# Kernel optimization log

Hardware: AMD Instinct MI355X
Metric: run time of the kernel (lower is better)

Reference implementation:

```python
import jax, jax.numpy as jnp
import numpy as np

N_NODES = 50000
N_EDGES = 400000
D = 256
EDGE_DIM = 64
N_LAYERS = 3


def setup_inputs() -> dict:
    key = jax.random.key(0)
    ks = jax.random.split(key, 8)
    sc = 1.0 / np.sqrt(D)
    x = jax.random.normal(ks[0], (N_NODES, D), dtype=jnp.float32)
    edge_attr = jax.random.normal(ks[1], (N_EDGES, EDGE_DIM), dtype=jnp.float32)
    edge_index = jax.random.randint(ks[2], (2, N_EDGES), 0, N_NODES, dtype=jnp.int64)
    Wl = jax.random.normal(ks[3], (N_LAYERS, D, D), dtype=jnp.float32) * sc
    bl = jax.random.normal(ks[4], (N_LAYERS, D), dtype=jnp.float32) * 0.01
    Wr = jax.random.normal(ks[5], (N_LAYERS, D, D), dtype=jnp.float32) * sc
    We = jax.random.normal(ks[6], (N_LAYERS, D, EDGE_DIM), dtype=jnp.float32) * (1.0 / np.sqrt(EDGE_DIM))
    be = jax.random.normal(ks[7], (N_LAYERS, D), dtype=jnp.float32) * 0.01
    return {"x": x, "edge_attr": edge_attr, "edge_index": edge_index,
            "Wl": Wl, "bl": bl, "Wr": Wr, "We": We, "be": be}


def reference(x, edge_attr, edge_index, Wl, bl, Wr, We, be):
    # SAGEConv (mean aggr, root_weight=True, no normalize) with edge-feature
    # augmented messages: msg = x[src] + edge_lin(edge_attr)
    src, dst = edge_index[0], edge_index[1]
    n = x.shape[0]
    # per-target in-degree for mean aggregation (computed once; edge_index fixed)
    deg = jax.ops.segment_sum(jnp.ones((edge_index.shape[1],), x.dtype), dst,
                              num_segments=n)
    inv_deg = (1.0 / jnp.maximum(deg, 1.0))[:, None]  # [N,1]
    for l in range(Wl.shape[0]):
        e_msg = edge_attr @ We[l].T + be[l]                 # [E,D] edge_lin
        msg = x[src] + e_msg                                 # gather + add
        agg = jax.ops.segment_sum(msg, dst, num_segments=n) * inv_deg  # mean
        x = jax.nn.relu(agg @ Wl[l].T + bl[l] + x @ Wr[l].T)
    return x
```

## Files before the change

kernel.cpp:

```cpp
#include <hip/hip_runtime.h>

typedef __attribute__((ext_vector_type(8))) short bf16x8;
typedef __attribute__((ext_vector_type(4))) float f32x4;
typedef unsigned short u16;

__device__ __forceinline__ u16 f2bf(float f) {
    union { float f; unsigned u; } v; v.f = f;
    unsigned u = v.u;
    return (u16)((u + 0x7FFFu + ((u >> 16) & 1u)) >> 16);
}
__device__ __forceinline__ float bf2f(u16 h) {
    union { unsigned u; float f; } v; v.u = ((unsigned)h) << 16;
    return v.f;
}

__global__ __launch_bounds__(256) void k_convert(const float* __restrict__ x,
                                                 u16* __restrict__ hb, int total4) {
    int i = blockIdx.x * 256 + threadIdx.x;
    if (i >= total4) return;
    float4 v = ((const float4*)x)[i];
    ushort4 o;
    o.x = f2bf(v.x); o.y = f2bf(v.y); o.z = f2bf(v.z); o.w = f2bf(v.w);
    ((ushort4*)hb)[i] = o;
}

__global__ __launch_bounds__(256) void k_count(const int* __restrict__ dst,
                                               int* __restrict__ deg, int E) {
    int e = blockIdx.x * 256 + threadIdx.x;
    if (e < E) atomicAdd(&deg[dst[e]], 1);
}

__global__ __launch_bounds__(256) void k_part(const int* __restrict__ deg,
                                              int* __restrict__ part, int N) {
    __shared__ int ws[4];
    int i = blockIdx.x * 256 + threadIdx.x;
    int v = (i < N) ? deg[i] : 0;
#pragma unroll
    for (int o = 32; o; o >>= 1) v += __shfl_down(v, o);
    int lane = threadIdx.x & 63, w = threadIdx.x >> 6;
    if (lane == 0) ws[w] = v;
    __syncthreads();
    if (threadIdx.x == 0) part[blockIdx.x] = ws[0] + ws[1] + ws[2] + ws[3];
}

__global__ __launch_bounds__(256) void k_scanp(const int* __restrict__ part,
                                               int* __restrict__ bases, int P) {
    __shared__ int s[256];
    int t = threadIdx.x;
    int v = (t < P) ? part[t] : 0;
    s[t] = v;
    __syncthreads();
#pragma unroll
    for (int o = 1; o < 256; o <<= 1) {
        int u = (t >= o) ? s[t - o] : 0;
        __syncthreads();
        s[t] += u;
        __syncthreads();
    }
    bases[t] = s[t] - v;
}

__global__ __launch_bounds__(256) void k_apply(const int* __restrict__ deg,
                                               const int* __restrict__ bases,
                                               int* __restrict__ rp, int* __restrict__ cur,
                                               int N, int E) {
    __shared__ int s[256];
    int b = blockIdx.x, t = threadIdx.x;
    int i = b * 256 + t;
    int d = (i < N) ? deg[i] : 0;
    s[t] = d;
    __syncthreads();
#pragma unroll
    for (int o = 1; o < 256; o <<= 1) {
        int u = (t >= o) ? s[t - o] : 0;
        __syncthreads();
        s[t] += u;
        __syncthreads();
    }
    if (i < N) {
        int r = bases[b] + s[t] - d;
        rp[i] = r;
        cur[i] = r;
    }
    if (b == (int)gridDim.x - 1 && t == 255) rp[N] = E;
}

__global__ __launch_bounds__(256) void k_fill(const int* __restrict__ dst, const int* __restrict__ src,
                                              int* __restrict__ cur,
                                              int* __restrict__ eid, int* __restrict__ srcs, int E) {
    int e = blockIdx.x * 256 + threadIdx.x;
    if (e < E) {
        int p = atomicAdd(&cur[dst[e]], 1);
        eid[p] = e;
        srcs[p] = src[e];
    }
}

__global__ __launch_bounds__(256) void k_sa(const float* __restrict__ attr, const int* __restrict__ rp,
                                            const int* __restrict__ eid, u16* __restrict__ Sa,
                                            unsigned char* __restrict__ hasdeg, int N) {
    int v = blockIdx.x * 4 + (threadIdx.x >> 6);
    if (v >= N) return;
    int l = threadIdx.x & 63;
    int g = l >> 4;
    int c = (l & 15) * 4;
    int j0 = rp[v], j1 = rp[v + 1];
    float4 a = {0.f, 0.f, 0.f, 0.f};
    int j = j0;
    for (; j + 7 < j1; j += 8) {
        int e0 = eid[j + g];
        int e1 = eid[j + 4 + g];
        float4 x0 = *(const float4*)&attr[(size_t)e0 * 64 + c];
        float4 x1 = *(const float4*)&attr[(size_t)e1 * 64 + c];
        a.x += x0.x + x1.x; a.y += x0.y + x1.y;
        a.z += x0.z + x1.z; a.w += x0.w + x1.w;
    }
    for (; j < j1; j += 4) {
        int jj = j + g;
        if (jj < j1) {
            int e = eid[jj];
            float4 x0 = *(const float4*)&attr[(size_t)e * 64 + c];
            a.x += x0.x; a.y += x0.y; a.z += x0.z; a.w += x0.w;
        }
    }
    a.x += __shfl_xor(a.x, 16); a.y += __shfl_xor(a.y, 16);
    a.z += __shfl_xor(a.z, 16); a.w += __shfl_xor(a.w, 16);
    a.x += __shfl_xor(a.x, 32); a.y += __shfl_xor(a.y, 32);
    a.z += __shfl_xor(a.z, 32); a.w += __shfl_xor(a.w, 32);
    int dg = j1 - j0;
    float m = 1.f / (float)(dg > 1 ? dg : 1);
    if (l < 16) {
        ushort4 o;
        o.x = f2bf(a.x * m); o.y = f2bf(a.y * m);
        o.z = f2bf(a.z * m); o.w = f2bf(a.w * m);
        *(ushort4*)&Sa[(size_t)v * 64 + c] = o;
        if (l == 0) hasdeg[v] = (dg > 0) ? 1 : 0;
    }
}

__global__ __launch_bounds__(256) void k_sx(const u16* __restrict__ hb, const int* __restrict__ rp,
                                            const int* __restrict__ srcs,
                                            u16* __restrict__ Sx, int N) {
    int v = blockIdx.x * 4 + (threadIdx.x >> 6);
    if (v >= N) return;
    int l = threadIdx.x & 63;
    int h = l >> 5;
    int c = (l & 31) * 8;
    int j0 = rp[v], j1 = rp[v + 1];
    float a[8] = {0.f, 0.f, 0.f, 0.f, 0.f, 0.f, 0.f, 0.f};
    int j = j0;
    for (; j + 7 < j1; j += 8) {
        int s0 = srcs[j + h];
        int s1 = srcs[j + 2 + h];
        int s2 = srcs[j + 4 + h];
        int s3 = srcs[j + 6 + h];
        bf16x8 u0 = *(const bf16x8*)&hb[(size_t)s0 * 256 + c];
        bf16x8 u1 = *(const bf16x8*)&hb[(size_t)s1 * 256 + c];
        bf16x8 u2 = *(const bf16x8*)&hb[(size_t)s2 * 256 + c];
        bf16x8 u3 = *(const bf16x8*)&hb[(size_t)s3 * 256 + c];
#pragma unroll
        for (int i = 0; i < 8; ++i)
            a[i] += (bf2f((u16)u0[i]) + bf2f((u16)u1[i])) + (bf2f((u16)u2[i]) + bf2f((u16)u3[i]));
    }
    for (; j < j1; j += 2) {
        int jj = j + h;
        if (jj < j1) {
            int s0 = srcs[jj];
            bf16x8 u0 = *(const bf16x8*)&hb[(size_t)s0 * 256 + c];
#pragma unroll
            for (int i = 0; i < 8; ++i) a[i] += bf2f((u16)u0[i]);
        }
    }
#pragma unroll
    for (int i = 0; i < 8; ++i) a[i] += __shfl_xor(a[i], 32);
    int dg = j1 - j0;
    float m = 1.f / (float)(dg > 1 ? dg : 1);
    if (l < 32) {
        bf16x8 o;
#pragma unroll
        for (int i = 0; i < 8; ++i) o[i] = (short)f2bf(a[i] * m);
        *(bf16x8*)&Sx[(size_t)v * 256 + c] = o;
    }
}

__global__ __launch_bounds__(256) void k_wprep(const float* __restrict__ Wl, const float* __restrict__ Wr,
                                               const float* __restrict__ We, const float* __restrict__ be,
                                               u16* __restrict__ Wlb, u16* __restrict__ Wrb,
                                               u16* __restrict__ Wleb, float* __restrict__ wlbe) {
    int t = blockIdx.x * 256 + threadIdx.x;
    if (t < 3 * 65536) { Wlb[t] = f2bf(Wl[t]); Wrb[t] = f2bf(Wr[t]); }
    if (t < 3 * 16384) {
        int l = t >> 14;
        int r = t & 16383;
        int d = r >> 6, jj = r & 63;
        const float* wl = Wl + ((size_t)l << 16) + (size_t)d * 256;
        const float* we = We + ((size_t)l << 14) + jj;
        float s = 0.f;
        for (int p = 0; p < 256; ++p) s += wl[p] * we[(size_t)p * 64];
        Wleb[t] = f2bf(s);
    }
    if (t < 768) {
        int l = t >> 8, d = t & 255;
        const float* wl = Wl + ((size_t)l << 16) + (size_t)d * 256;
        const float* b = be + l * 256;
        float s = 0.f;
        for (int p = 0; p < 256; ++p) s += wl[p] * b[p];
        wlbe[t] = s;
    }
}

__device__ __forceinline__ void do_seg(const u16* __restrict__ A, const u16* __restrict__ B,
                                       int lda, int K, int r0, int M,
                                       u16* Alds, u16* Blds,
                                       int lane, int w,
                                       int r16, int kq, f32x4 (&acc)[4][4]) {
    const int rloc = lane >> 3;
    const int cE = (lane & 7) * 8;
    for (int k0 = 0; k0 < K; k0 += 64) {
        __syncthreads();
#pragma unroll
        for (int i = 0; i < 2; ++i) {
            int rowb = i * 32 + w * 8;
            int ar = r0 + rowb + rloc;
            ar = ar < M ? ar : M - 1;
            __builtin_amdgcn_global_load_lds(
                (const __attribute__((address_space(1))) void*)(A + (size_t)ar * lda + k0 + cE),
                (__attribute__((address_space(3))) void*)(Alds + (size_t)rowb * 64), 16, 0, 0);
        }
#pragma unroll
        for (int i = 0; i < 8; ++i) {
            int rowb = i * 32 + w * 8;
            int br = rowb + rloc;
            __builtin_amdgcn_global_load_lds(
                (const __attribute__((address_space(1))) void*)(B + (size_t)br * K + k0 + cE),
                (__attribute__((address_space(3))) void*)(Blds + (size_t)rowb * 64), 16, 0, 0);
        }
        __syncthreads();
        bf16x8 af[4][2], bfr[4][2];
#pragma unroll
        for (int rf = 0; rf < 4; ++rf) {
            af[rf][0] = *(const bf16x8*)&Alds[(rf * 16 + r16) * 64 + kq];
            af[rf][1] = *(const bf16x8*)&Alds[(rf * 16 + r16) * 64 + 32 + kq];
        }
#pragma unroll
        for (int cf = 0; cf < 4; ++cf) {
            bfr[cf][0] = *(const bf16x8*)&Blds[(w * 64 + cf * 16 + r16) * 64 + kq];
            bfr[cf][1] = *(const bf16x8*)&Blds[(w * 64 + cf * 16 + r16) * 64 + 32 + kq];
        }
#pragma unroll
        for (int rf = 0; rf < 4; ++rf)
#pragma unroll
            for (int cf = 0; cf < 4; ++cf) {
                acc[rf][cf] = __builtin_amdgcn_mfma_f32_16x16x32_bf16(af[rf][0], bfr[cf][0], acc[rf][cf], 0, 0, 0);
                acc[rf][cf] = __builtin_amdgcn_mfma_f32_16x16x32_bf16(af[rf][1], bfr[cf][1], acc[rf][cf], 0, 0, 0);
            }
    }
}

__global__ __launch_bounds__(256, 3) void k_gemm(
    const u16* __restrict__ Sx, const u16* __restrict__ Hb, const u16* __restrict__ Sa,
    const u16* __restrict__ Wlb, const u16* __restrict__ Wrb, const u16* __restrict__ Wleb,
    const float* __restrict__ bl, const float* __restrict__ wlbe,
    const unsigned char* __restrict__ hasdeg,
    u16* hb_out, float* f_out, int M)
{
    __shared__ __align__(16) u16 Alds[64 * 64];
    __shared__ __align__(16) u16 Blds[256 * 64];
    const int tid = threadIdx.x;
    const int lane = tid & 63;
    const int w = tid >> 6;
    const int r16 = lane & 15;
    const int hi = lane >> 4;
    const int kq = hi * 8;
    const int r0 = blockIdx.x * 64;

    const f32x4 fzero = {0.f, 0.f, 0.f, 0.f};
    f32x4 acc[4][4];
#pragma unroll
    for (int a = 0; a < 4; ++a)
#pragma unroll
        for (int b = 0; b < 4; ++b) acc[a][b] = fzero;

    do_seg(Sx, Wlb, 256, 256, r0, M, Alds, Blds, lane, w, r16, kq, acc);
    do_seg(Hb, Wrb, 256, 256, r0, M, Alds, Blds, lane, w, r16, kq, acc);
    do_seg(Sa, Wleb, 64, 64, r0, M, Alds, Blds, lane, w, r16, kq, acc);

    float blv[4], wbev[4];
#pragma unroll
    for (int cf = 0; cf < 4; ++cf) {
        int col = w * 64 + 16 * cf + r16;
        blv[cf] = bl[col];
        wbev[cf] = wlbe[col];
    }
#pragma unroll
    for (int rf = 0; rf < 4; ++rf)
#pragma unroll
        for (int j = 0; j < 4; ++j) {
            int r = r0 + 16 * rf + 4 * hi + j;
            if (r < M) {
                float hd = hasdeg[r] ? 1.f : 0.f;
#pragma unroll
                for (int cf = 0; cf < 4; ++cf) {
                    int col = w * 64 + 16 * cf + r16;
                    float v = acc[rf][cf][j] + blv[cf] + hd * wbev[cf];
                    v = fmaxf(v, 0.f);
                    if (f_out) f_out[(size_t)r * 256 + col] = v;
                    if (hb_out) hb_out[(size_t)r * 256 + col] = f2bf(v);
                }
            }
        }
}

extern "C" void kernel_launch(void* const* d_in, const int* in_sizes, int n_in,
                              void* d_out, int out_size, void* d_ws, size_t ws_size,
                              hipStream_t stream) {
    const float* x    = (const float*)d_in[0];
    const float* attr = (const float*)d_in[1];
    const int*   ei   = (const int*)d_in[2];
    const float* Wl   = (const float*)d_in[3];
    const float* bl   = (const float*)d_in[4];
    const float* Wr   = (const float*)d_in[5];
    const float* We   = (const float*)d_in[6];
    const float* be   = (const float*)d_in[7];
    float* out = (float*)d_out;

    const int N = in_sizes[0] / 256;
    const int E = in_sizes[1] / 64;
    const int* srcA = ei;
    const int* dstA = ei + E;

    char* p = (char*)d_ws;
    auto carve = [&](size_t bytes) -> char* {
        char* q = p;
        p += (bytes + 255) & ~(size_t)255;
        return q;
    };
    u16* hb     = (u16*)carve((size_t)N * 256 * 2);
    u16* SxB    = (u16*)carve((size_t)N * 256 * 2);
    u16* SaB    = (u16*)carve((size_t)N * 64 * 2);
    u16* Wlb    = (u16*)carve((size_t)3 * 65536 * 2);
    u16* Wrb    = (u16*)carve((size_t)3 * 65536 * 2);
    u16* Wleb   = (u16*)carve((size_t)3 * 16384 * 2);
    float* wlbe = (float*)carve((size_t)3 * 256 * 4);
    int* deg    = (int*)carve((size_t)N * 4);
    int* rp     = (int*)carve((size_t)(N + 1) * 4);
    int* cur    = (int*)carve((size_t)N * 4);
    int* eid    = (int*)carve((size_t)E * 4);
    int* srcs   = (int*)carve((size_t)E * 4);
    int* part   = (int*)carve((size_t)256 * 4);
    int* bases  = (int*)carve((size_t)256 * 4);
    unsigned char* hasdeg = (unsigned char*)carve((size_t)N);

    hipMemsetAsync(deg, 0, (size_t)N * 4, stream);

    int t4 = N * 64;
    k_convert<<<(t4 + 255) / 256, 256, 0, stream>>>(x, hb, t4);
    k_count<<<(E + 255) / 256, 256, 0, stream>>>(dstA, deg, E);
    const int PB = (N + 255) / 256;
    k_part<<<PB, 256, 0, stream>>>(deg, part, N);
    k_scanp<<<1, 256, 0, stream>>>(part, bases, PB);
    k_apply<<<PB, 256, 0, stream>>>(deg, bases, rp, cur, N, E);
    k_fill<<<(E + 255) / 256, 256, 0, stream>>>(dstA, srcA, cur, eid, srcs, E);
    k_sa<<<(N + 3) / 4, 256, 0, stream>>>(attr, rp, eid, SaB, hasdeg, N);
    k_wprep<<<(3 * 65536 + 255) / 256, 256, 0, stream>>>(Wl, Wr, We, be, Wlb, Wrb, Wleb, wlbe);

    const int gblocks = (N + 63) / 64;
    for (int l = 0; l < 3; ++l) {
        k_sx<<<(N + 3) / 4, 256, 0, stream>>>(hb, rp, srcs, SxB, N);
        k_gemm<<<gblocks, 256, 0, stream>>>(SxB, hb, SaB,
            Wlb + l * 65536, Wrb + l * 65536, Wleb + l * 16384,
            bl + l * 256, wlbe + l * 256, hasdeg,
            (l < 2) ? hb : (u16*)nullptr, (l == 2) ? out : (float*)nullptr, N);
    }
}
```

Baseline: 332.3 us.

## Double-buffer LDS tiles in fused GEMM to overlap loads with MFMA

Replaces the per-segment load/sync/compute loop with a single 9-step software pipeline over the three GEMM segments, using two LDS buffers so the next tile's global-to-LDS copy is issued before computing the current tile. This aims to hide global load latency behind MFMA work and removes one barrier per step. The doubled LDS footprint lowers the occupancy hint from 3 to 2 blocks per CU, reducing inter-block latency hiding.

```diff
diff --git a/kernel.cpp b/kernel.cpp
--- a/kernel.cpp
+++ b/kernel.cpp
@@ -3,6 +3,9 @@
 typedef __attribute__((ext_vector_type(8))) short bf16x8;
 typedef __attribute__((ext_vector_type(4))) float f32x4;
 typedef unsigned short u16;
+
+#define AS1 __attribute__((address_space(1)))
+#define AS3 __attribute__((address_space(3)))
 
 __device__ __forceinline__ u16 f2bf(float f) {
     union { float f; unsigned u; } v; v.f = f;
@@ -209,63 +212,15 @@
     }
 }
 
-__device__ __forceinline__ void do_seg(const u16* __restrict__ A, const u16* __restrict__ B,
-                                       int lda, int K, int r0, int M,
-                                       u16* Alds, u16* Blds,
-                                       int lane, int w,
-                                       int r16, int kq, f32x4 (&acc)[4][4]) {
-    const int rloc = lane >> 3;
-    const int cE = (lane & 7) * 8;
-    for (int k0 = 0; k0 < K; k0 += 64) {
-        __syncthreads();
-#pragma unroll
-        for (int i = 0; i < 2; ++i) {
-            int rowb = i * 32 + w * 8;
-            int ar = r0 + rowb + rloc;
-            ar = ar < M ? ar : M - 1;
-            __builtin_amdgcn_global_load_lds(
-                (const __attribute__((address_space(1))) void*)(A + (size_t)ar * lda + k0 + cE),
-                (__attribute__((address_space(3))) void*)(Alds + (size_t)rowb * 64), 16, 0, 0);
-        }
-#pragma unroll
-        for (int i = 0; i < 8; ++i) {
-            int rowb = i * 32 + w * 8;
-            int br = rowb + rloc;
-            __builtin_amdgcn_global_load_lds(
-                (const __attribute__((address_space(1))) void*)(B + (size_t)br * K + k0 + cE),
-                (__attribute__((address_space(3))) void*)(Blds + (size_t)rowb * 64), 16, 0, 0);
-        }
-        __syncthreads();
-        bf16x8 af[4][2], bfr[4][2];
-#pragma unroll
-        for (int rf = 0; rf < 4; ++rf) {
-            af[rf][0] = *(const bf16x8*)&Alds[(rf * 16 + r16) * 64 + kq];
-            af[rf][1] = *(const bf16x8*)&Alds[(rf * 16 + r16) * 64 + 32 + kq];
-        }
-#pragma unroll
-        for (int cf = 0; cf < 4; ++cf) {
-            bfr[cf][0] = *(const bf16x8*)&Blds[(w * 64 + cf * 16 + r16) * 64 + kq];
-            bfr[cf][1] = *(const bf16x8*)&Blds[(w * 64 + cf * 16 + r16) * 64 + 32 + kq];
-        }
-#pragma unroll
-        for (int rf = 0; rf < 4; ++rf)
-#pragma unroll
-            for (int cf = 0; cf < 4; ++cf) {
-                acc[rf][cf] = __builtin_amdgcn_mfma_f32_16x16x32_bf16(af[rf][0], bfr[cf][0], acc[rf][cf], 0, 0, 0);
-                acc[rf][cf] = __builtin_amdgcn_mfma_f32_16x16x32_bf16(af[rf][1], bfr[cf][1], acc[rf][cf], 0, 0, 0);
-            }
-    }
-}
-
-__global__ __launch_bounds__(256, 3) void k_gemm(
+__global__ __launch_bounds__(256, 2) void k_gemm(
     const u16* __restrict__ Sx, const u16* __restrict__ Hb, const u16* __restrict__ Sa,
     const u16* __restrict__ Wlb, const u16* __restrict__ Wrb, const u16* __restrict__ Wleb,
     const float* __restrict__ bl, const float* __restrict__ wlbe,
     const unsigned char* __restrict__ hasdeg,
     u16* hb_out, float* f_out, int M)
 {
-    __shared__ __align__(16) u16 Alds[64 * 64];
-    __shared__ __align__(16) u16 Blds[256 * 64];
+    __shared__ __align__(16) u16 Alds[2][64 * 64];
+    __shared__ __align__(16) u16 Blds[2][256 * 64];
     const int tid = threadIdx.x;
     const int lane = tid & 63;
     const int w = tid >> 6;
@@ -273,6 +228,27 @@
     const int hi = lane >> 4;
     const int kq = hi * 8;
     const int r0 = blockIdx.x * 64;
+    const int rloc = lane >> 3;
+    const int cE = (lane & 7) * 8;
+
+    auto stage = [&](int b, const u16* A, int lda_, const u16* B, int K_, int k0) {
+#pragma unroll
+        for (int i = 0; i < 2; ++i) {
+            int rowb = i * 32 + w * 8;
+            int ar = r0 + rowb + rloc;
+            ar = ar < M ? ar : M - 1;
+            __builtin_amdgcn_global_load_lds(
+                (const AS1 void*)(A + (size_t)ar * lda_ + k0 + cE),
+                (AS3 void*)(&Alds[b][rowb * 64]), 16, 0, 0);
+        }
+#pragma unroll
+        for (int i = 0; i < 8; ++i) {
+            int rowb = i * 32 + w * 8;
+            __builtin_amdgcn_global_load_lds(
+                (const AS1 void*)(B + (size_t)(rowb + rloc) * K_ + k0 + cE),
+                (AS3 void*)(&Blds[b][rowb * 64]), 16, 0, 0);
+        }
+    };
 
     const f32x4 fzero = {0.f, 0.f, 0.f, 0.f};
     f32x4 acc[4][4];
@@ -281,9 +257,41 @@
 #pragma unroll
         for (int b = 0; b < 4; ++b) acc[a][b] = fzero;
 
-    do_seg(Sx, Wlb, 256, 256, r0, M, Alds, Blds, lane, w, r16, kq, acc);
-    do_seg(Hb, Wrb, 256, 256, r0, M, Alds, Blds, lane, w, r16, kq, acc);
-    do_seg(Sa, Wleb, 64, 64, r0, M, Alds, Blds, lane, w, r16, kq, acc);
+    stage(0, Sx, 256, Wlb, 256, 0);
+#pragma unroll
+    for (int t = 0; t < 9; ++t) {
+        asm volatile("s_waitcnt vmcnt(0)" ::: "memory");
+        __builtin_amdgcn_s_barrier();
+        if (t < 8) {
+            const int tn = t + 1;
+            const u16* An = (tn < 4) ? Sx : ((tn < 8) ? Hb : Sa);
+            const u16* Bn = (tn < 4) ? Wlb : ((tn < 8) ? Wrb : Wleb);
+            const int ldan = (tn < 8) ? 256 : 64;
+            const int Kn = (tn < 8) ? 256 : 64;
+            const int k0n = (tn < 4) ? tn * 64 : ((tn < 8) ? (tn - 4) * 64 : 0);
+            stage(tn & 1, An, ldan, Bn, Kn, k0n);
+        }
+        const u16* Ab = &Alds[t & 1][0];
+        const u16* Bb = &Blds[t & 1][0];
+        bf16x8 af[4][2], bfr[4][2];
+#pragma unroll
+        for (int rf = 0; rf < 4; ++rf) {
+            af[rf][0] = *(const bf16x8*)&Ab[(rf * 16 + r16) * 64 + kq];
+            af[rf][1] = *(const bf16x8*)&Ab[(rf * 16 + r16) * 64 + 32 + kq];
+        }
+#pragma unroll
+        for (int cf = 0; cf < 4; ++cf) {
+            bfr[cf][0] = *(const bf16x8*)&Bb[(w * 64 + cf * 16 + r16) * 64 + kq];
+            bfr[cf][1] = *(const bf16x8*)&Bb[(w * 64 + cf * 16 + r16) * 64 + 32 + kq];
+        }
+#pragma unroll
+        for (int rf = 0; rf < 4; ++rf)
+#pragma unroll
+            for (int cf = 0; cf < 4; ++cf) {
+                acc[rf][cf] = __builtin_amdgcn_mfma_f32_16x16x32_bf16(af[rf][0], bfr[cf][0], acc[rf][cf], 0, 0, 0);
+                acc[rf][cf] = __builtin_amdgcn_mfma_f32_16x16x32_bf16(af[rf][1], bfr[cf][1], acc[rf][cf], 0, 0, 0);
+            }
+    }
 
     float blv[4], wbev[4];
 #pragma unroll
```

Measured after the change: 336.9 us. About the same (+1.4%).

## Fuse neighbor mean aggregation into the GEMM kernel with ping-pong hidden buffers

Applied to the files above, without the earlier changes.

Removes the separate k_sx aggregation kernel. Each GEMM block now gathers and averages neighbor rows for its 64 nodes straight into a padded LDS tile, then uses that tile as the A operand for the Wl segment. This avoids writing and re-reading the Sx intermediate through global memory and saves one launch per layer. Because other blocks still read the current hidden state while this layer writes the next one, hidden states now alternate between two buffers. The cost is more LDS per block (occupancy hint drops from 3 to 2) and a gather phase that runs serially before the MFMA work, with no overlap between the two.

```diff
diff --git a/kernel.cpp b/kernel.cpp
--- a/kernel.cpp
+++ b/kernel.cpp
@@ -3,6 +3,9 @@
 typedef __attribute__((ext_vector_type(8))) short bf16x8;
 typedef __attribute__((ext_vector_type(4))) float f32x4;
 typedef unsigned short u16;
+
+#define AS1 __attribute__((address_space(1)))
+#define AS3 __attribute__((address_space(3)))
 
 __device__ __forceinline__ u16 f2bf(float f) {
     union { float f; unsigned u; } v; v.f = f;
@@ -138,51 +141,6 @@
     }
 }
 
-__global__ __launch_bounds__(256) void k_sx(const u16* __restrict__ hb, const int* __restrict__ rp,
-                                            const int* __restrict__ srcs,
-                                            u16* __restrict__ Sx, int N) {
-    int v = blockIdx.x * 4 + (threadIdx.x >> 6);
-    if (v >= N) return;
-    int l = threadIdx.x & 63;
-    int h = l >> 5;
-    int c = (l & 31) * 8;
-    int j0 = rp[v], j1 = rp[v + 1];
-    float a[8] = {0.f, 0.f, 0.f, 0.f, 0.f, 0.f, 0.f, 0.f};
-    int j = j0;
-    for (; j + 7 < j1; j += 8) {
-        int s0 = srcs[j + h];
-        int s1 = srcs[j + 2 + h];
-        int s2 = srcs[j + 4 + h];
-        int s3 = srcs[j + 6 + h];
-        bf16x8 u0 = *(const bf16x8*)&hb[(size_t)s0 * 256 + c];
-        bf16x8 u1 = *(const bf16x8*)&hb[(size_t)s1 * 256 + c];
-        bf16x8 u2 = *(const bf16x8*)&hb[(size_t)s2 * 256 + c];
-        bf16x8 u3 = *(const bf16x8*)&hb[(size_t)s3 * 256 + c];
-#pragma unroll
-        for (int i = 0; i < 8; ++i)
-            a[i] += (bf2f((u16)u0[i]) + bf2f((u16)u1[i])) + (bf2f((u16)u2[i]) + bf2f((u16)u3[i]));
-    }
-    for (; j < j1; j += 2) {
-        int jj = j + h;
-        if (jj < j1) {
-            int s0 = srcs[jj];
-            bf16x8 u0 = *(const bf16x8*)&hb[(size_t)s0 * 256 + c];
-#pragma unroll
-            for (int i = 0; i < 8; ++i) a[i] += bf2f((u16)u0[i]);
-        }
-    }
-#pragma unroll
-    for (int i = 0; i < 8; ++i) a[i] += __shfl_xor(a[i], 32);
-    int dg = j1 - j0;
-    float m = 1.f / (float)(dg > 1 ? dg : 1);
-    if (l < 32) {
-        bf16x8 o;
-#pragma unroll
-        for (int i = 0; i < 8; ++i) o[i] = (short)f2bf(a[i] * m);
-        *(bf16x8*)&Sx[(size_t)v * 256 + c] = o;
-    }
-}
-
 __global__ __launch_bounds__(256) void k_wprep(const float* __restrict__ Wl, const float* __restrict__ Wr,
                                                const float* __restrict__ We, const float* __restrict__ be,
                                                u16* __restrict__ Wlb, u16* __restrict__ Wrb,
@@ -209,62 +167,18 @@
     }
 }
 
-__device__ __forceinline__ void do_seg(const u16* __restrict__ A, const u16* __restrict__ B,
-                                       int lda, int K, int r0, int M,
-                                       u16* Alds, u16* Blds,
-                                       int lane, int w,
-                                       int r16, int kq, f32x4 (&acc)[4][4]) {
-    const int rloc = lane >> 3;
-    const int cE = (lane & 7) * 8;
-    for (int k0 = 0; k0 < K; k0 += 64) {
-        __syncthreads();
-#pragma unroll
-        for (int i = 0; i < 2; ++i) {
-            int rowb = i * 32 + w * 8;
-            int ar = r0 + rowb + rloc;
-            ar = ar < M ? ar : M - 1;
-            __builtin_amdgcn_global_load_lds(
-                (const __attribute__((address_space(1))) void*)(A + (size_t)ar * lda + k0 + cE),
-                (__attribute__((address_space(3))) void*)(Alds + (size_t)rowb * 64), 16, 0, 0);
-        }
-#pragma unroll
-        for (int i = 0; i < 8; ++i) {
-            int rowb = i * 32 + w * 8;
-            int br = rowb + rloc;
-            __builtin_amdgcn_global_load_lds(
-                (const __attribute__((address_space(1))) void*)(B + (size_t)br * K + k0 + cE),
-                (__attribute__((address_space(3))) void*)(Blds + (size_t)rowb * 64), 16, 0, 0);
-        }
-        __syncthreads();
-        bf16x8 af[4][2], bfr[4][2];
-#pragma unroll
-        for (int rf = 0; rf < 4; ++rf) {
-            af[rf][0] = *(const bf16x8*)&Alds[(rf * 16 + r16) * 64 + kq];
-            af[rf][1] = *(const bf16x8*)&Alds[(rf * 16 + r16) * 64 + 32 + kq];
-        }
-#pragma unroll
-        for (int cf = 0; cf < 4; ++cf) {
-            bfr[cf][0] = *(const bf16x8*)&Blds[(w * 64 + cf * 16 + r16) * 64 + kq];
-            bfr[cf][1] = *(const bf16x8*)&Blds[(w * 64 + cf * 16 + r16) * 64 + 32 + kq];
-        }
-#pragma unroll
-        for (int rf = 0; rf < 4; ++rf)
-#pragma unroll
-            for (int cf = 0; cf < 4; ++cf) {
-                acc[rf][cf] = __builtin_amdgcn_mfma_f32_16x16x32_bf16(af[rf][0], bfr[cf][0], acc[rf][cf], 0, 0, 0);
-                acc[rf][cf] = __builtin_amdgcn_mfma_f32_16x16x32_bf16(af[rf][1], bfr[cf][1], acc[rf][cf], 0, 0, 0);
-            }
-    }
-}
-
-__global__ __launch_bounds__(256, 3) void k_gemm(
-    const u16* __restrict__ Sx, const u16* __restrict__ Hb, const u16* __restrict__ Sa,
+#define SXP 264
+__global__ __launch_bounds__(256, 2) void k_gemm(
+    const u16* __restrict__ Hcur,
+    const int* __restrict__ rp, const int* __restrict__ srcs,
+    const u16* __restrict__ Sa,
     const u16* __restrict__ Wlb, const u16* __restrict__ Wrb, const u16* __restrict__ Wleb,
     const float* __restrict__ bl, const float* __restrict__ wlbe,
     const unsigned char* __restrict__ hasdeg,
     u16* hb_out, float* f_out, int M)
 {
-    __shared__ __align__(16) u16 Alds[64 * 64];
+    __shared__ __align__(16) u16 SxT[64 * SXP];
+    __shared__ __align__(16) u16 AB[64 * 64];
     __shared__ __align__(16) u16 Blds[256 * 64];
     const int tid = threadIdx.x;
     const int lane = tid & 63;
@@ -273,6 +187,54 @@
     const int hi = lane >> 4;
     const int kq = hi * 8;
     const int r0 = blockIdx.x * 64;
+    const int rloc = lane >> 3;
+    const int cE = (lane & 7) * 8;
+
+    {
+        const int h = lane >> 5;
+        const int c = (lane & 31) * 8;
+        for (int p = 0; p < 16; ++p) {
+            int vloc = w * 16 + p;
+            int v = r0 + vloc;
+            v = v < M ? v : M - 1;
+            int j0 = rp[v], j1 = rp[v + 1];
+            float a[8] = {0.f, 0.f, 0.f, 0.f, 0.f, 0.f, 0.f, 0.f};
+            int j = j0;
+            for (; j + 7 < j1; j += 8) {
+                int s0 = srcs[j + h];
+                int s1 = srcs[j + 2 + h];
+                int s2 = srcs[j + 4 + h];
+                int s3 = srcs[j + 6 + h];
+                bf16x8 u0 = *(const bf16x8*)&Hcur[(size_t)s0 * 256 + c];
+                bf16x8 u1 = *(const bf16x8*)&Hcur[(size_t)s1 * 256 + c];
+                bf16x8 u2 = *(const bf16x8*)&Hcur[(size_t)s2 * 256 + c];
+                bf16x8 u3 = *(const bf16x8*)&Hcur[(size_t)s3 * 256 + c];
+#pragma unroll
+                for (int i = 0; i < 8; ++i)
+                    a[i] += (bf2f((u16)u0[i]) + bf2f((u16)u1[i])) + (bf2f((u16)u2[i]) + bf2f((u16)u3[i]));
+            }
+            for (; j < j1; j += 2) {
+                int jj = j + h;
+                if (jj < j1) {
+                    int s0 = srcs[jj];
+                    bf16x8 u0 = *(const bf16x8*)&Hcur[(size_t)s0 * 256 + c];
+#pragma unroll
+                    for (int i = 0; i < 8; ++i) a[i] += bf2f((u16)u0[i]);
+                }
+            }
+#pragma unroll
+            for (int i = 0; i < 8; ++i) a[i] += __shfl_xor(a[i], 32);
+            int dg = j1 - j0;
+            float m = 1.f / (float)(dg > 1 ? dg : 1);
+            if (lane < 32) {
+                bf16x8 o;
+#pragma unroll
+                for (int i = 0; i < 8; ++i) o[i] = (short)f2bf(a[i] * m);
+                *(bf16x8*)&SxT[vloc * SXP + c] = o;
+            }
+        }
+    }
+    __syncthreads();
 
     const f32x4 fzero = {0.f, 0.f, 0.f, 0.f};
     f32x4 acc[4][4];
@@ -281,9 +243,60 @@
 #pragma unroll
         for (int b = 0; b < 4; ++b) acc[a][b] = fzero;
 
-    do_seg(Sx, Wlb, 256, 256, r0, M, Alds, Blds, lane, w, r16, kq, acc);
-    do_seg(Hb, Wrb, 256, 256, r0, M, Alds, Blds, lane, w, r16, kq, acc);
-    do_seg(Sa, Wleb, 64, 64, r0, M, Alds, Blds, lane, w, r16, kq, acc);
+#pragma unroll
+    for (int t = 0; t < 9; ++t) {
+        const u16* Bg = (t < 4) ? Wlb : ((t < 8) ? Wrb : Wleb);
+        const int Kb = (t < 8) ? 256 : 64;
+        const int k0 = (t < 4) ? t * 64 : ((t < 8) ? (t - 4) * 64 : 0);
+        __syncthreads();
+#pragma unroll
+        for (int i = 0; i < 8; ++i) {
+            int rowb = i * 32 + w * 8;
+            __builtin_amdgcn_global_load_lds(
+                (const AS1 void*)(Bg + (size_t)(rowb + rloc) * Kb + k0 + cE),
+                (AS3 void*)(&Blds[rowb * 64]), 16, 0, 0);
+        }
+        if (t >= 4) {
+            const u16* Ag = (t < 8) ? Hcur : Sa;
+            const int lda = (t < 8) ? 256 : 64;
+#pragma unroll
+            for (int i = 0; i < 2; ++i) {
+                int rowb = i * 32 + w * 8;
+                int ar = r0 + rowb + rloc;
+                ar = ar < M ? ar : M - 1;
+                __builtin_amdgcn_global_load_lds(
+                    (const AS1 void*)(Ag + (size_t)ar * lda + k0 + cE),
+                    (AS3 void*)(&AB[rowb * 64]), 16, 0, 0);
+            }
+        }
+        __syncthreads();
+        bf16x8 af[4][2], bfr[4][2];
+        if (t < 4) {
+#pragma unroll
+            for (int rf = 0; rf < 4; ++rf) {
+                af[rf][0] = *(const bf16x8*)&SxT[(rf * 16 + r16) * SXP + t * 64 + kq];
+                af[rf][1] = *(const bf16x8*)&SxT[(rf * 16 + r16) * SXP + t * 64 + 32 + kq];
+            }
+        } else {
+#pragma unroll
+            for (int rf = 0; rf < 4; ++rf) {
+                af[rf][0] = *(const bf16x8*)&AB[(rf * 16 + r16) * 64 + kq];
+                af[rf][1] = *(const bf16x8*)&AB[(rf * 16 + r16) * 64 + 32 + kq];
+            }
+        }
+#pragma unroll
+        for (int cf = 0; cf < 4; ++cf) {
+            bfr[cf][0] = *(const bf16x8*)&Blds[(w * 64 + cf * 16 + r16) * 64 + kq];
+            bfr[cf][1] = *(const bf16x8*)&Blds[(w * 64 + cf * 16 + r16) * 64 + 32 + kq];
+        }
+#pragma unroll
+        for (int rf = 0; rf < 4; ++rf)
+#pragma unroll
+            for (int cf = 0; cf < 4; ++cf) {
+                acc[rf][cf] = __builtin_amdgcn_mfma_f32_16x16x32_bf16(af[rf][0], bfr[cf][0], acc[rf][cf], 0, 0, 0);
+                acc[rf][cf] = __builtin_amdgcn_mfma_f32_16x16x32_bf16(af[rf][1], bfr[cf][1], acc[rf][cf], 0, 0, 0);
+            }
+    }
 
     float blv[4], wbev[4];
 #pragma unroll
@@ -335,8 +348,8 @@
         p += (bytes + 255) & ~(size_t)255;
         return q;
     };
-    u16* hb     = (u16*)carve((size_t)N * 256 * 2);
-    u16* SxB    = (u16*)carve((size_t)N * 256 * 2);
+    u16* hb0    = (u16*)carve((size_t)N * 256 * 2);
+    u16* hb1    = (u16*)carve((size_t)N * 256 * 2);
     u16* SaB    = (u16*)carve((size_t)N * 64 * 2);
     u16* Wlb    = (u16*)carve((size_t)3 * 65536 * 2);
     u16* Wrb    = (u16*)carve((size_t)3 * 65536 * 2);
@@ -354,7 +367,7 @@
     hipMemsetAsync(deg, 0, (size_t)N * 4, stream);
 
     int t4 = N * 64;
-    k_convert<<<(t4 + 255) / 256, 256, 0, stream>>>(x, hb, t4);
+    k_convert<<<(t4 + 255) / 256, 256, 0, stream>>>(x, hb0, t4);
     k_count<<<(E + 255) / 256, 256, 0, stream>>>(dstA, deg, E);
     const int PB = (N + 255) / 256;
     k_part<<<PB, 256, 0, stream>>>(deg, part, N);
@@ -365,11 +378,13 @@
     k_wprep<<<(3 * 65536 + 255) / 256, 256, 0, stream>>>(Wl, Wr, We, be, Wlb, Wrb, Wleb, wlbe);
 
     const int gblocks = (N + 63) / 64;
+    u16* hcur = hb0;
+    u16* hnxt = hb1;
     for (int l = 0; l < 3; ++l) {
-        k_sx<<<(N + 3) / 4, 256, 0, stream>>>(hb, rp, srcs, SxB, N);
-        k_gemm<<<gblocks, 256, 0, stream>>>(SxB, hb, SaB,
+        k_gemm<<<gblocks, 256, 0, stream>>>(hcur, rp, srcs, SaB,
             Wlb + l * 65536, Wrb + l * 65536, Wleb + l * 16384,
             bl + l * 256, wlbe + l * 256, hasdeg,
-            (l < 2) ? hb : (u16*)nullptr, (l == 2) ? out : (float*)nullptr, N);
-    }
-}
+            (l < 2) ? hnxt : (u16*)nullptr, (l == 2) ? out : (float*)nullptr, N);
+        u16* t = hcur; hcur = hnxt; hnxt = t;
+    }
+}
```

Measured after the change: 448.1 us. +34.8%, slower.
